# Kernel tuning notes

Hardware: AMD Instinct MI355X
Metric: run time of the kernel (lower is better)

The kernel has to match this reference:

```python
import jax, jax.numpy as jnp
import numpy as np

SCALE = 2
PAD = 4
EPS = 1e-5
K = 5
N, C, H, W = 4, 64, 128, 128


def _splits(a, s):
    # (..., W, H) -> (..., W/s, H/s, s*s), block decimation matching torch view/permute
    *lead, Wd, Hd = a.shape
    b = a.reshape(*lead, s, Wd // s, s, Hd // s)
    nl = len(lead)
    b = jnp.transpose(b, tuple(range(nl)) + (nl + 1, nl + 3, nl, nl + 2))
    return b.reshape(*lead, Wd // s, Hd // s, s * s)


def _p2o(psf, Hs, Ws):
    # PSF -> OTF: zero-pad, roll to center at origin, FFT
    kh, kw = psf.shape[-2], psf.shape[-1]
    otf = jnp.zeros(psf.shape[:-2] + (Hs, Ws), psf.dtype).at[..., :kh, :kw].set(psf)
    otf = jnp.roll(otf, (-(kh // 2), -(kw // 2)), axis=(-2, -1))
    return jnp.fft.fftn(otf, axes=(-2, -1))


def _upsample(x, s):
    # s-fold zero-filling upsampler (S^T y)
    n, c, h, w = x.shape
    return jnp.zeros((n, c, h * s, w * s), x.dtype).at[..., ::s, ::s].set(x)


def setup_inputs() -> dict:
    key = jax.random.key(0)
    kx, kw_, _ = jax.random.split(key, 3)
    x = jax.random.normal(kx, (N, C, H, W), dtype=jnp.float32)
    w_raw = jax.random.normal(kw_, (1, C, K, K), dtype=jnp.float32)
    weight = jax.nn.softmax(w_raw.reshape(1, C, -1), axis=-1).reshape(1, C, K, K)
    bias = jnp.zeros((1, C, 1, 1), dtype=jnp.float32)
    return {"x": x, "weight": weight, "bias": bias}


def reference(x, weight, bias):
    s = SCALE
    xp = jnp.pad(x, ((0, 0), (0, 0), (PAD, PAD), (PAD, PAD)), mode="wrap")  # circular
    biaseps = jax.nn.sigmoid(bias - 9.0) + EPS  # (1,C,1,1)
    _, _, h, w = xp.shape
    STy = _upsample(xp, s)  # zero-filled upsample
    # nearest-neighbor interpolate by integer factor s
    xn = jnp.repeat(jnp.repeat(xp, s, axis=-2), s, axis=-1)
    FB = _p2o(weight, h * s, w * s)           # (1,C,hs,ws) complex
    FBC = jnp.conj(FB)
    F2B = jnp.abs(FB) ** 2                     # real
    FBFy = FBC * jnp.fft.fftn(STy, axes=(-2, -1))
    FR = FBFy + jnp.fft.fftn(biaseps * xn, axes=(-2, -1))
    x1 = FB * FR
    FBR = jnp.mean(_splits(x1, s), axis=-1)    # (N,C,h,w) complex
    invW = jnp.mean(_splits(F2B, s), axis=-1)  # (1,C,h,w) real
    invWBR = FBR / (invW + biaseps)
    FCBinvWBR = FBC * jnp.tile(invWBR, (1, 1, s, s))
    FX = (FR - FCBinvWBR) / biaseps
    out = jnp.real(jnp.fft.ifftn(FX, axes=(-2, -1)))
    out = out[..., PAD * s:-PAD * s, PAD * s:-PAD * s]
    return out
```

## Files before the change

kernel.cpp:

```cpp
#include <hip/hip_runtime.h>
#include <math.h>


#define MDIM 136
#define RSC  70
#define HC   69
#define PLANE_HALF (MDIM*HC)
#define NPLANES 256
#define LDS_CPLX2 (2*MDIM*RSC + 2*MDIM + 2*119 + 2*51)
#define PI_D 3.14159265358979323846
#define NTH 1024

__device__ __forceinline__ int slot136(int k) { return 17*(k & 7) + (k >> 3); }
__device__ __forceinline__ int slot68(int k)  { return 17*(k & 3) + (k >> 2); }

template<int DIR, class F>
__device__ __forceinline__ void dft17_sink(float2* z, int base, int stride, F f)
{
    constexpr float C17[9] = {1.f, 0.93247223f, 0.73900892f, 0.44573836f,
                              0.09226836f, -0.27366299f, -0.60263464f,
                              -0.85021714f, -0.98297310f};
    constexpr float S17[9] = {0.f, 0.36124167f, 0.67369564f, 0.89516329f,
                              0.99573418f, 0.96182564f, 0.79801723f,
                              0.52643216f, 0.18374952f};
    constexpr float d = (DIR > 0) ? 1.f : -1.f;
    float xr[17], xi[17];
#pragma unroll
    for (int n = 0; n < 17; n++) {
        float2 v = z[base + n*stride];
        xr[n] = v.x; xi[n] = v.y;
    }
    float ar[8], ai[8], br[8], bi[8];
#pragma unroll
    for (int n = 1; n <= 8; n++) {
        ar[n-1] = xr[n] + xr[17-n];  ai[n-1] = xi[n] + xi[17-n];
        br[n-1] = xr[n] - xr[17-n];  bi[n-1] = xi[n] - xi[17-n];
    }
    float s0r = xr[0], s0i = xi[0];
#pragma unroll
    for (int n = 0; n < 8; n++) { s0r += ar[n]; s0i += ai[n]; }
    f(0, s0r, s0i);
#pragma unroll
    for (int k = 1; k <= 8; k++) {
        float Pr = xr[0], Pi = xi[0], Qr = 0.f, Qi = 0.f;
#pragma unroll
        for (int n = 1; n <= 8; n++) {
            int m = (k*n) % 17;
            float cc = (m <= 8) ? C17[m] : C17[17-m];
            float ss = (m <= 8) ? S17[m] : -S17[17-m];
            Pr = fmaf(ar[n-1], cc, Pr);
            Pi = fmaf(ai[n-1], cc, Pi);
            Qr = fmaf(br[n-1], ss, Qr);
            Qi = fmaf(bi[n-1], ss, Qi);
        }
        f(k,    Pr - d*Qi, Pi + d*Qr);
        f(17-k, Pr + d*Qi, Pi - d*Qr);
    }
}

template<int DIR>
__device__ __forceinline__ void radix4_tw(float2* z, const float2* t68, int base, int n2,
                                          float2 Z0, float2 Z1, float2 Z2, float2 Z3)
{
    constexpr float d = (DIR > 0) ? 1.0f : -1.0f;
    float t0r = Z0.x+Z2.x, t0i = Z0.y+Z2.y;
    float t1r = Z0.x-Z2.x, t1i = Z0.y-Z2.y;
    float t2r = Z1.x+Z3.x, t2i = Z1.y+Z3.y;
    float t3r = Z1.x-Z3.x, t3i = Z1.y-Z3.y;
    float X0r = t0r+t2r,     X0i = t0i+t2i;
    float X2r = t0r-t2r,     X2i = t0i-t2i;
    float X1r = t1r - d*t3i, X1i = t1i + d*t3r;
    float X3r = t1r + d*t3i, X3i = t1i - d*t3r;
    z[base + n2] = make_float2(X0r, X0i);
    float2 w1 = t68[n2], w2 = t68[17 + n2], w3 = t68[34 + n2];
    z[base + 17 + n2] = make_float2(X1r*w1.x - X1i*w1.y, X1r*w1.y + X1i*w1.x);
    z[base + 34 + n2] = make_float2(X2r*w2.x - X2i*w2.y, X2r*w2.y + X2i*w2.x);
    z[base + 51 + n2] = make_float2(X3r*w3.x - X3i*w3.y, X3r*w3.y + X3i*w3.x);
}

template<int DIR>
__device__ __forceinline__ void fft136_s1_body(float2* z, const float2* t136,
                                               int c, int n2)
{
    constexpr float d = (DIR > 0) ? 1.0f : -1.0f;
    constexpr float C707 = 0.70710678118654752f;
    float xr[8], xi[8];
#pragma unroll
    for (int n1 = 0; n1 < 8; n1++) {
        float2 v = z[(17*n1 + n2)*RSC + c];
        xr[n1] = v.x; xi[n1] = v.y;
    }
    float e0r = xr[0]+xr[4], e0i = xi[0]+xi[4];
    float e1r = xr[0]-xr[4], e1i = xi[0]-xi[4];
    float o0r = xr[2]+xr[6], o0i = xi[2]+xi[6];
    float o1r = xr[2]-xr[6], o1i = xi[2]-xi[6];
    float E0r = e0r+o0r, E0i = e0i+o0i;
    float E2r = e0r-o0r, E2i = e0i-o0i;
    float E1r = e1r - d*o1i, E1i = e1i + d*o1r;
    float E3r = e1r + d*o1i, E3i = e1i - d*o1r;
    float f0r = xr[1]+xr[5], f0i = xi[1]+xi[5];
    float f1r = xr[1]-xr[5], f1i = xi[1]-xi[5];
    float h0r = xr[3]+xr[7], h0i = xi[3]+xi[7];
    float h1r = xr[3]-xr[7], h1i = xi[3]-xi[7];
    float O0r = f0r+h0r, O0i = f0i+h0i;
    float O2r = f0r-h0r, O2i = f0i-h0i;
    float O1r = f1r - d*h1i, O1i = f1i + d*h1r;
    float O3r = f1r + d*h1i, O3i = f1i - d*h1r;
    float t1r =  C707*(O1r - d*O1i), t1i = C707*(O1i + d*O1r);
    float t2r = -d*O2i,              t2i = d*O2r;
    float t3r = -C707*(O3r + d*O3i), t3i = C707*(d*O3r - O3i);
    float Xr[8], Xi[8];
    Xr[0]=E0r+O0r; Xi[0]=E0i+O0i;  Xr[4]=E0r-O0r; Xi[4]=E0i-O0i;
    Xr[1]=E1r+t1r; Xi[1]=E1i+t1i;  Xr[5]=E1r-t1r; Xi[5]=E1i-t1i;
    Xr[2]=E2r+t2r; Xi[2]=E2i+t2i;  Xr[6]=E2r-t2r; Xi[6]=E2i-t2i;
    Xr[3]=E3r+t3r; Xi[3]=E3i+t3i;  Xr[7]=E3r-t3r; Xi[7]=E3i-t3i;
    z[n2*RSC + c] = make_float2(Xr[0], Xi[0]);
#pragma unroll
    for (int k1 = 1; k1 < 8; k1++) {
        float2 w = t136[(k1-1)*17 + n2];
        z[(17*k1 + n2)*RSC + c] = make_float2(Xr[k1]*w.x - Xi[k1]*w.y,
                                              Xr[k1]*w.y + Xi[k1]*w.x);
    }
}

template<int DIR>
__device__ void fft136_s1(float2* z, const float2* t136, int ncols, int tid)
{
    int c = tid / 17;
    int n2 = tid - c*17;
    for (int e = tid; e < ncols*17; e += NTH) {
        fft136_s1_body<DIR>(z, t136, c, n2);
        c += 60; n2 += 4; if (n2 >= 17) { n2 -= 17; c++; }
    }
}

template<int DIR>
__device__ void ct68_s1(float2* z, const float2* t68, int tid)
{
    int row = tid / 17;
    int n2  = tid - row*17;
    for (int e = tid; e < MDIM*17; e += NTH) {
        int base = row*RSC;
        float2 Z0 = z[base + n2];
        float2 Z1 = z[base + 17 + n2];
        float2 Z2 = z[base + 34 + n2];
        float2 Z3 = z[base + 51 + n2];
        radix4_tw<DIR>(z, t68, base, n2, Z0, Z1, Z2, Z3);
        row += 60; n2 += 4; if (n2 >= 17) { n2 -= 17; row++; }
    }
}

__device__ __forceinline__ float2 c2r_pack(float2 a, float2 b, float2 w)
{
    float Sr = a.x + b.x, Si = a.y - b.y;
    float Dr = a.x - b.x, Di = a.y + b.y;
    float Or = w.x*Dr - w.y*Di, Oi = w.x*Di + w.y*Dr;
    return make_float2(Sr - Oi, Si + Or);
}

__global__ __launch_bounds__(1024, 4) void conv_kernel(const float* __restrict__ x,
                                                       const float2* __restrict__ Abuf,
                                                       float* __restrict__ out)
{
    extern __shared__ float2 zsm[];
    float2* z0    = zsm;
    float2* z1    = zsm + MDIM*RSC;
    float2* lutI  = zsm + 2*MDIM*RSC;
    float2* lutF  = lutI + MDIM;
    float2* tI136 = lutF + MDIM;
    float2* tF136 = tI136 + 119;
    float2* tI68  = tF136 + 119;
    float2* tF68  = tI68 + 51;
    const int tid = threadIdx.x;
    const int nc  = blockIdx.x;
    const int c   = nc & 63;

    if (tid < MDIM) {
        float s, cc; sincosf(2.0f*(float)PI_D*(float)tid/136.0f, &s, &cc);
        lutI[tid] = make_float2(cc, s);
        lutF[tid] = make_float2(cc, -s);
    } else if (tid < MDIM + 119) {
        int it = tid - MDIM;
        int k1 = it/17 + 1, n2 = it - (it/17)*17;
        float s, cc; sincosf((float)(PI_D/68.0)*(float)(k1*n2), &s, &cc);
        tI136[it] = make_float2(cc, s);
        tF136[it] = make_float2(cc, -s);
    } else if (tid < MDIM + 119 + 51) {
        int it = tid - MDIM - 119;
        int j = it/17, n2 = it - 17*j;
        float s, cc; sincosf((float)(PI_D/34.0)*(float)((j+1)*n2), &s, &cc);
        tI68[it] = make_float2(cc, s);
        tF68[it] = make_float2(cc, -s);
    }
    const float* xp = x + (size_t)nc * (128*128);
    {
        int i = tid / 68, n = tid - (tid/68)*68;
        for (int e = tid; e < MDIM*68; e += NTH) {
            int si = (i + 124) & 127;
            int j0 = (2*n + 124) & 127;
            z0[i*RSC + n] = *reinterpret_cast<const float2*>(xp + si*128 + j0);
            i += 15; n += 4; if (n >= 68) { n -= 68; i++; }
        }
    }
    __syncthreads();
    ct68_s1<-1>(z0, tF68, tid);
    __syncthreads();
    if (tid < MDIM*4) {
        int row = tid >> 2, k1 = tid & 3;
        int base = row*RSC + 17*k1;
        dft17_sink<-1>(z0, base, 1, [&](int k2, float re, float im) {
            z0[base + k2] = make_float2(re, im);
        });
    }
    __syncthreads();
    {
        int row = tid / 35, k = tid - (tid/35)*35;
        for (int e = tid; e < MDIM*35; e += NTH) {
            int base = row*RSC;
            int sa = slot68(k);
            float2 Za = z0[base+sa];
            float Zar = Za.x, Zai = Za.y;
            float Zbr, Zbi; int sb;
            if (k == 0) { Zbr = Zar; Zbi = Zai; sb = 68; }
            else {
                int kk = 68-k; sb = slot68(kk);
                float2 Zb = z0[base+sb]; Zbr = Zb.x; Zbi = Zb.y;
            }
            float2 w = lutF[k];
            float wc = w.x, ws = w.y;
            float Er = 0.5f*(Zar + Zbr), Ei = 0.5f*(Zai - Zbi);
            float Dr = 0.5f*(Zar - Zbr), Di = 0.5f*(Zai + Zbi);
            float Tr = wc*Dr - ws*Di, Ti = wc*Di + ws*Dr;
            z0[base+sa] = make_float2(Er + Ti, Ei - Tr);
            float E2r = Er,  E2i = -Ei;
            float D2r = -Dr, D2i = Di;
            float w2c = -wc, w2s = ws;
            float T2r = w2c*D2r - w2s*D2i, T2i = w2c*D2i + w2s*D2r;
            z0[base+sb] = make_float2(E2r + T2i, E2i - T2r);
            row += 29; k += 9; if (k >= 35) { k -= 35; row++; }
        }
    }
    __syncthreads();
    float2 Ar0[10], Ar1[10];
    {
        const float2* A0 = Abuf + (size_t)(c*4) * PLANE_HALF;
        const float2* A1 = A0 + PLANE_HALF;
        int e = tid;
#pragma unroll
        for (int k = 0; k < 10; k++) {
            if (k < 9 || tid < PLANE_HALF - 9*NTH) { Ar0[k] = A0[e]; Ar1[k] = A1[e]; }
            e += NTH;
        }
    }
    fft136_s1<-1>(z0, tF136, HC, tid);
    __syncthreads();
    if (tid < HC*8) {
        int cc = tid >> 3, k1 = tid & 7;
        int base = 17*k1*RSC + cc;
        dft17_sink<-1>(z0, base, RSC, [&](int k2, float re, float im) {
            z0[base + k2*RSC] = make_float2(re, im);
        });
    }
    __syncthreads();
    float2 Xreg[10];
    {
        int g1 = tid / HC, g2 = tid - (tid/HC)*HC;
#pragma unroll
        for (int k = 0; k < 10; k++) {
            if (k < 9 || tid < PLANE_HALF - 9*NTH) {
                int cq = (g2 == 68) ? 68 : slot68(g2);
                Xreg[k] = z0[slot136(g1)*RSC + cq];
            }
            g1 += 14; g2 += 58; if (g2 >= HC) { g2 -= HC; g1++; }
        }
    }
    __syncthreads();
    float* op = out + (size_t)nc * (256*256);
#pragma unroll 1
    for (int u = 0; u < 2; u++) {
        {
            int g1 = tid / HC, g2 = tid - (tid/HC)*HC;
#pragma unroll
            for (int k = 0; k < 10; k++) {
                if (k < 9 || tid < PLANE_HALF - 9*NTH) {
                    float2 xv = Xreg[k];
                    float2 a0 = Ar0[k], a1 = Ar1[k];
                    int a = g1*RSC + g2;
                    z0[a] = make_float2(a0.x*xv.x - a0.y*xv.y, a0.x*xv.y + a0.y*xv.x);
                    z1[a] = make_float2(a1.x*xv.x - a1.y*xv.y, a1.x*xv.y + a1.y*xv.x);
                }
                g1 += 14; g2 += 58; if (g2 >= HC) { g2 -= HC; g1++; }
            }
        }
        __syncthreads();
        if (u == 0) {
            const float2* A0 = Abuf + (size_t)(c*4 + 2) * PLANE_HALF;
            const float2* A1 = A0 + PLANE_HALF;
            int e = tid;
#pragma unroll
            for (int k = 0; k < 10; k++) {
                if (k < 9 || tid < PLANE_HALF - 9*NTH) { Ar0[k] = A0[e]; Ar1[k] = A1[e]; }
                e += NTH;
            }
        }
        for (int it = tid; it < 2*HC*17; it += NTH) {
            int pl = it >= HC*17;
            int ee = it - (pl ? HC*17 : 0);
            int cc = (ee*241) >> 12;
            int n2 = ee - cc*17;
            fft136_s1_body<1>(pl ? z1 : z0, tI136, cc, n2);
        }
        __syncthreads();
        for (int it = tid; it < 2*HC*8; it += NTH) {
            int pl = it >= HC*8;
            int i  = it - (pl ? HC*8 : 0);
            float2* zz = pl ? z1 : z0;
            int cc = i >> 3, k1 = i & 7;
            int base = 17*k1*RSC + cc;
            dft17_sink<1>(zz, base, RSC, [&](int k2, float re, float im) {
                zz[base + k2*RSC] = make_float2(re, im);
            });
        }
        __syncthreads();
        for (int it = tid; it < 2*MDIM*9; it += NTH) {
            int pl = it >= MDIM*9;
            int i  = it - (pl ? MDIM*9 : 0);
            float2* zz = pl ? z1 : z0;
            int row = (i*7282) >> 16;
            int g   = i - row*9;
            int base = row*RSC;
            if (g == 0) {
                float2 T0  = zz[base],    T17 = zz[base+17], T34 = zz[base+34],
                       T51 = zz[base+51], T68 = zz[base+68];
                float2 Z0 = c2r_pack(T0,  T68, lutI[0]);
                float2 Z1 = c2r_pack(T17, T51, lutI[17]);
                float2 Z2 = c2r_pack(T34, T34, lutI[34]);
                float2 Z3 = c2r_pack(T51, T17, lutI[51]);
                radix4_tw<1>(zz, tI68, base, 0, Z0, Z1, Z2, Z3);
            } else {
                int gb = 17 - g;
                float2 Ta0 = zz[base+g],    Ta1 = zz[base+g+17],
                       Ta2 = zz[base+g+34], Ta3 = zz[base+g+51];
                float2 Tb0 = zz[base+gb],    Tb1 = zz[base+gb+17],
                       Tb2 = zz[base+gb+34], Tb3 = zz[base+gb+51];
                float2 Za0 = c2r_pack(Ta0, Tb3, lutI[g]);
                float2 Za1 = c2r_pack(Ta1, Tb2, lutI[g+17]);
                float2 Za2 = c2r_pack(Ta2, Tb1, lutI[g+34]);
                float2 Za3 = c2r_pack(Ta3, Tb0, lutI[g+51]);
                float2 Zb0 = c2r_pack(Tb0, Ta3, lutI[gb]);
                float2 Zb1 = c2r_pack(Tb1, Ta2, lutI[gb+17]);
                float2 Zb2 = c2r_pack(Tb2, Ta1, lutI[gb+34]);
                float2 Zb3 = c2r_pack(Tb3, Ta0, lutI[gb+51]);
                radix4_tw<1>(zz, tI68, base, g,  Za0, Za1, Za2, Za3);
                radix4_tw<1>(zz, tI68, base, gb, Zb0, Zb1, Zb2, Zb3);
            }
        }
        __syncthreads();
        for (int it = tid; it < 2*MDIM*4; it += NTH) {
            int pl = it >= MDIM*4;
            int i  = it - (pl ? MDIM*4 : 0);
            float2* zz = pl ? z1 : z0;
            int row = i >> 2, k1 = i & 3;
            int base = row*RSC + 17*k1;
            dft17_sink<1>(zz, base, 1, [&](int k2, float re, float im) {
                zz[base + k2] = make_float2(re, im);
            });
        }
        __syncthreads();
        {
            int m  = 2 + (tid & 63);
            int y1 = 4 + (tid >> 6);
            int a  = slot136(y1)*RSC + slot68(m);
            float* rowp = op + (size_t)(2*y1 + u - 8)*256 + 4*m - 8;
#pragma unroll
            for (int it = 0; it < 8; ++it) {
                float2 w0 = z0[a], w1 = z1[a];
                *reinterpret_cast<float4*>(rowp) = make_float4(w0.x, w1.x, w0.y, w1.y);
                a += 2*RSC;
                rowp += 32*256;
            }
        }
        __syncthreads();
    }
}

__global__ void prep_kernel(const float* __restrict__ weight,
                            const float* __restrict__ bias,
                            float2* __restrict__ Abuf)
{
    __shared__ double tabc[272], tabs[272];
    __shared__ double Rs[69*5*4];
    for (int t = threadIdx.x; t < 272; t += blockDim.x) {
        double s, c; sincos(-2.0*PI_D*(double)t/272.0, &s, &c);
        tabc[t] = c; tabs[t] = s;
    }
    const int c     = blockIdx.x >> 3;
    const int chunk = blockIdx.x & 7;
    const float* wp = weight + c*25;
    const double r = 1.0/(1.0 + exp(9.0 - (double)bias[c])) + 1e-5;
    __syncthreads();
    for (int it = threadIdx.x; it < 69*5; it += blockDim.x) {
        int g2 = it / 5, a = it - 5*g2;
        double c2 = tabc[g2], s2 = tabs[g2];
        double e2r[5], e2i[5];
        e2r[2]=1.0; e2i[2]=0.0; e2r[3]=c2; e2i[3]=s2;
        e2r[4]=c2*c2-s2*s2; e2i[4]=2.0*c2*s2;
        e2r[1]=c2; e2i[1]=-s2; e2r[0]=e2r[4]; e2i[0]=-e2i[4];
        double w0=wp[a*5+0], w1=wp[a*5+1], w2=wp[a*5+2], w3=wp[a*5+3], w4=wp[a*5+4];
        double Rer = w0*e2r[0] + w2*e2r[2] + w4*e2r[4];
        double Rei = w0*e2i[0] + w2*e2i[2] + w4*e2i[4];
        double Ror = w1*e2r[1] + w3*e2r[3];
        double Roi = w1*e2i[1] + w3*e2i[3];
        Rs[it*4+0] = Rer + Ror;  Rs[it*4+1] = Rei + Roi;
        Rs[it*4+2] = Rer - Ror;  Rs[it*4+3] = Rei - Roi;
    }
    __syncthreads();

    const int e_lo = chunk * 1173;
    const int e_hi = e_lo + 1173;
    int e  = e_lo + (int)threadIdx.x;
    int g1 = e / HC, g2 = e - (e/HC)*HC;
    for (; e < e_hi; e += blockDim.x) {
        double c1 = tabc[g1], s1 = tabs[g1];
        double e1r[5], e1i[5];
        e1r[2]=1.0; e1i[2]=0.0; e1r[3]=c1; e1i[3]=s1;
        e1r[4]=c1*c1-s1*s1; e1i[4]=2.0*c1*s1;
        e1r[1]=c1; e1i[1]=-s1; e1r[0]=e1r[4]; e1i[0]=-e1i[4];

        double FBr[2][2], FBi[2][2];
#pragma unroll
        for (int b1 = 0; b1 < 2; b1++) {
            double Per=0, Pei=0, Por=0, Poi=0;
#pragma unroll
            for (int a = 0; a < 5; a++) {
                double Rr = Rs[(g2*5+a)*4 + 2*b1];
                double Ri = Rs[(g2*5+a)*4 + 2*b1 + 1];
                double tr = e1r[a]*Rr - e1i[a]*Ri;
                double ti = e1r[a]*Ri + e1i[a]*Rr;
                if (a & 1) { Por += tr; Poi += ti; } else { Per += tr; Pei += ti; }
            }
            FBr[0][b1] = Per + Por;  FBi[0][b1] = Pei + Poi;
            FBr[1][b1] = Per - Por;  FBi[1][b1] = Pei - Poi;
        }
        double c2 = tabc[g2], s2 = tabs[g2];
        double ur[2]={1.0+c1, 1.0-c1}, ui[2]={s1, -s1};
        double vr[2]={1.0+c2, 1.0-c2}, vi[2]={s2, -s2};
        double Br_[2][2], Bi_[2][2];
#pragma unroll
        for (int a1 = 0; a1 < 2; a1++)
#pragma unroll
            for (int b1 = 0; b1 < 2; b1++) {
                Br_[a1][b1] = ur[a1]*vr[b1] - ui[a1]*vi[b1];
                Bi_[a1][b1] = ur[a1]*vi[b1] + ui[a1]*vr[b1];
            }
        double invW=0, Qr=0, Qi=0;
#pragma unroll
        for (int a1 = 0; a1 < 2; a1++)
#pragma unroll
            for (int b1 = 0; b1 < 2; b1++) {
                invW += FBr[a1][b1]*FBr[a1][b1] + FBi[a1][b1]*FBi[a1][b1];
                Qr += FBr[a1][b1]*Br_[a1][b1] - FBi[a1][b1]*Bi_[a1][b1];
                Qi += FBr[a1][b1]*Bi_[a1][b1] + FBi[a1][b1]*Br_[a1][b1];
            }
        invW *= 0.25; Qr *= 0.25; Qi *= 0.25;
        double den = 1.0/(invW + r);
        double Sr = (1.0 - Qr)*den, Si = -Qi*den;
        double Mr[2][2], Mi[2][2];
#pragma unroll
        for (int a1 = 0; a1 < 2; a1++)
#pragma unroll
            for (int b1 = 0; b1 < 2; b1++) {
                Mr[a1][b1] = Br_[a1][b1] + FBr[a1][b1]*Sr + FBi[a1][b1]*Si;
                Mi[a1][b1] = Bi_[a1][b1] + FBr[a1][b1]*Si - FBi[a1][b1]*Sr;
            }
        const double scale = 1.0/73984.0;
#pragma unroll
        for (int uu = 0; uu < 2; uu++)
#pragma unroll
            for (int vv = 0; vv < 2; vv++) {
                double sr=0, si=0;
#pragma unroll
                for (int a1 = 0; a1 < 2; a1++)
#pragma unroll
                    for (int b1 = 0; b1 < 2; b1++) {
                        if ((a1*uu + b1*vv) & 1) { sr -= Mr[a1][b1]; si -= Mi[a1][b1]; }
                        else                     { sr += Mr[a1][b1]; si += Mi[a1][b1]; }
                    }
                int t = g1*uu + g2*vv;
                double pc = tabc[t], ps = -tabs[t];
                float2 outv;
                outv.x = (float)((pc*sr - ps*si)*scale);
                outv.y = (float)((pc*si + ps*sr)*scale);
                Abuf[((size_t)(c*4 + uu*2 + vv))*PLANE_HALF + e] = outv;
            }
        g1 += 3; g2 += 49; if (g2 >= HC) { g2 -= HC; g1++; }
    }
}

extern "C" void kernel_launch(void* const* d_in, const int* in_sizes, int n_in,
                              void* d_out, int out_size, void* d_ws, size_t ws_size,
                              hipStream_t stream)
{
    const float* x      = (const float*)d_in[0];
    const float* weight = (const float*)d_in[1];
    const float* bias   = (const float*)d_in[2];
    float* out = (float*)d_out;

    float2* Abuf = (float2*)d_ws;

    const size_t lds_conv = (size_t)LDS_CPLX2 * sizeof(float2);
    (void)hipFuncSetAttribute((const void*)conv_kernel,
                              hipFuncAttributeMaxDynamicSharedMemorySize, (int)lds_conv);

    prep_kernel<<<512, 256, 0, stream>>>(weight, bias, Abuf);
    conv_kernel<<<NPLANES, 1024, lds_conv, stream>>>(x, Abuf, out);
}
```

Before: 153.8 us.

## Interleave the two inverse-FFT planes into float4 LDS layout

The two output-phase planes (v=0,1) are stored interleaved as one float4 per element in LDS and in the precomputed filter buffer, instead of two separate float2 planes. The inverse FFT stages then process both planes in a single pass with 128-bit LDS accesses, which halves the number of butterfly iterations and index computations. Filter coefficients are now loaded from global memory as float4 inside the u loop rather than prefetched into registers, which lowers register pressure but exposes that load latency. The forward FFT keeps using the first half of the same buffer through a float2 view with a doubled row stride.

```diff
diff --git a/kernel.cpp b/kernel.cpp
--- a/kernel.cpp
+++ b/kernel.cpp
@@ -3,16 +3,32 @@
 
 
 #define MDIM 136
-#define RSC  70
+#define RSCF 140
+#define RSC4 70
 #define HC   69
 #define PLANE_HALF (MDIM*HC)
 #define NPLANES 256
-#define LDS_CPLX2 (2*MDIM*RSC + 2*MDIM + 2*119 + 2*51)
+#define LDS_BYTES (MDIM*RSC4*16 + 612*8)
 #define PI_D 3.14159265358979323846
 #define NTH 1024
 
 __device__ __forceinline__ int slot136(int k) { return 17*(k & 7) + (k >> 3); }
 __device__ __forceinline__ int slot68(int k)  { return 17*(k & 3) + (k >> 2); }
+
+__device__ __forceinline__ float4 q_add(float4 a, float4 b)
+{ return make_float4(a.x+b.x, a.y+b.y, a.z+b.z, a.w+b.w); }
+__device__ __forceinline__ float4 q_sub(float4 a, float4 b)
+{ return make_float4(a.x-b.x, a.y-b.y, a.z-b.z, a.w-b.w); }
+__device__ __forceinline__ float4 q_muli(float4 a, float d)
+{ return make_float4(-d*a.y, d*a.x, -d*a.w, d*a.z); }
+__device__ __forceinline__ float4 q_scale(float4 a, float s)
+{ return make_float4(s*a.x, s*a.y, s*a.z, s*a.w); }
+__device__ __forceinline__ float4 q_fma(float4 a, float s, float4 acc)
+{ return make_float4(fmaf(a.x,s,acc.x), fmaf(a.y,s,acc.y),
+                     fmaf(a.z,s,acc.z), fmaf(a.w,s,acc.w)); }
+__device__ __forceinline__ float4 cmul4(float4 q, float2 w)
+{ return make_float4(q.x*w.x - q.y*w.y, q.x*w.y + q.y*w.x,
+                     q.z*w.x - q.w*w.y, q.z*w.y + q.w*w.x); }
 
 template<int DIR, class F>
 __device__ __forceinline__ void dft17_sink(float2* z, int base, int stride, F f)
@@ -55,6 +71,46 @@
         }
         f(k,    Pr - d*Qi, Pi + d*Qr);
         f(17-k, Pr + d*Qi, Pi - d*Qr);
+    }
+}
+
+template<int DIR>
+__device__ __forceinline__ void dft17q(float4* z, int base, int stride)
+{
+    constexpr float C17[9] = {1.f, 0.93247223f, 0.73900892f, 0.44573836f,
+                              0.09226836f, -0.27366299f, -0.60263464f,
+                              -0.85021714f, -0.98297310f};
+    constexpr float S17[9] = {0.f, 0.36124167f, 0.67369564f, 0.89516329f,
+                              0.99573418f, 0.96182564f, 0.79801723f,
+                              0.52643216f, 0.18374952f};
+    constexpr float d = (DIR > 0) ? 1.f : -1.f;
+    float4 x0 = z[base];
+    float4 a[8], b[8];
+#pragma unroll
+    for (int n = 1; n <= 8; n++) {
+        float4 u = z[base + n*stride];
+        float4 v = z[base + (17-n)*stride];
+        a[n-1] = q_add(u, v);
+        b[n-1] = q_sub(u, v);
+    }
+    float4 s0 = x0;
+#pragma unroll
+    for (int n = 0; n < 8; n++) s0 = q_add(s0, a[n]);
+    z[base] = s0;
+#pragma unroll
+    for (int k = 1; k <= 8; k++) {
+        float4 P = x0, Q = make_float4(0.f,0.f,0.f,0.f);
+#pragma unroll
+        for (int n = 1; n <= 8; n++) {
+            int m = (k*n) % 17;
+            float cc = (m <= 8) ? C17[m] : C17[17-m];
+            float ss = (m <= 8) ? S17[m] : -S17[17-m];
+            P = q_fma(a[n-1], cc, P);
+            Q = q_fma(b[n-1], ss, Q);
+        }
+        float4 iq = q_muli(Q, d);
+        z[base + k*stride]      = q_add(P, iq);
+        z[base + (17-k)*stride] = q_sub(P, iq);
     }
 }
 
@@ -79,6 +135,23 @@
 }
 
 template<int DIR>
+__device__ __forceinline__ void radix4q_tw(float4* z, const float2* t68, int base, int n2,
+                                           float4 Z0, float4 Z1, float4 Z2, float4 Z3)
+{
+    constexpr float d = (DIR > 0) ? 1.0f : -1.0f;
+    float4 t0 = q_add(Z0, Z2), t1 = q_sub(Z0, Z2);
+    float4 t2 = q_add(Z1, Z3), t3 = q_sub(Z1, Z3);
+    float4 X0 = q_add(t0, t2), X2 = q_sub(t0, t2);
+    float4 it3 = q_muli(t3, d);
+    float4 X1 = q_add(t1, it3), X3 = q_sub(t1, it3);
+    z[base + n2] = X0;
+    float2 w1 = t68[n2], w2 = t68[17 + n2], w3 = t68[34 + n2];
+    z[base + 17 + n2] = cmul4(X1, w1);
+    z[base + 34 + n2] = cmul4(X2, w2);
+    z[base + 51 + n2] = cmul4(X3, w3);
+}
+
+template<int DIR>
 __device__ __forceinline__ void fft136_s1_body(float2* z, const float2* t136,
                                                int c, int n2)
 {
@@ -87,7 +160,7 @@
     float xr[8], xi[8];
 #pragma unroll
     for (int n1 = 0; n1 < 8; n1++) {
-        float2 v = z[(17*n1 + n2)*RSC + c];
+        float2 v = z[(17*n1 + n2)*RSCF + c];
         xr[n1] = v.x; xi[n1] = v.y;
     }
     float e0r = xr[0]+xr[4], e0i = xi[0]+xi[4];
@@ -114,40 +187,49 @@
     Xr[1]=E1r+t1r; Xi[1]=E1i+t1i;  Xr[5]=E1r-t1r; Xi[5]=E1i-t1i;
     Xr[2]=E2r+t2r; Xi[2]=E2i+t2i;  Xr[6]=E2r-t2r; Xi[6]=E2i-t2i;
     Xr[3]=E3r+t3r; Xi[3]=E3i+t3i;  Xr[7]=E3r-t3r; Xi[7]=E3i-t3i;
-    z[n2*RSC + c] = make_float2(Xr[0], Xi[0]);
+    z[n2*RSCF + c] = make_float2(Xr[0], Xi[0]);
 #pragma unroll
     for (int k1 = 1; k1 < 8; k1++) {
         float2 w = t136[(k1-1)*17 + n2];
-        z[(17*k1 + n2)*RSC + c] = make_float2(Xr[k1]*w.x - Xi[k1]*w.y,
-                                              Xr[k1]*w.y + Xi[k1]*w.x);
+        z[(17*k1 + n2)*RSCF + c] = make_float2(Xr[k1]*w.x - Xi[k1]*w.y,
+                                               Xr[k1]*w.y + Xi[k1]*w.x);
     }
 }
 
 template<int DIR>
-__device__ void fft136_s1(float2* z, const float2* t136, int ncols, int tid)
-{
-    int c = tid / 17;
-    int n2 = tid - c*17;
-    for (int e = tid; e < ncols*17; e += NTH) {
-        fft136_s1_body<DIR>(z, t136, c, n2);
-        c += 60; n2 += 4; if (n2 >= 17) { n2 -= 17; c++; }
-    }
-}
-
-template<int DIR>
-__device__ void ct68_s1(float2* z, const float2* t68, int tid)
-{
-    int row = tid / 17;
-    int n2  = tid - row*17;
-    for (int e = tid; e < MDIM*17; e += NTH) {
-        int base = row*RSC;
-        float2 Z0 = z[base + n2];
-        float2 Z1 = z[base + 17 + n2];
-        float2 Z2 = z[base + 34 + n2];
-        float2 Z3 = z[base + 51 + n2];
-        radix4_tw<DIR>(z, t68, base, n2, Z0, Z1, Z2, Z3);
-        row += 60; n2 += 4; if (n2 >= 17) { n2 -= 17; row++; }
-    }
+__device__ __forceinline__ void fft136q_s1_body(float4* z, const float2* t136,
+                                                int c, int n2)
+{
+    constexpr float d = (DIR > 0) ? 1.0f : -1.0f;
+    constexpr float C707 = 0.70710678118654752f;
+    float4 x[8];
+#pragma unroll
+    for (int n1 = 0; n1 < 8; n1++) x[n1] = z[(17*n1 + n2)*RSC4 + c];
+    float4 e0 = q_add(x[0], x[4]), e1 = q_sub(x[0], x[4]);
+    float4 o0 = q_add(x[2], x[6]), o1 = q_sub(x[2], x[6]);
+    float4 E0 = q_add(e0, o0), E2 = q_sub(e0, o0);
+    float4 io1 = q_muli(o1, d);
+    float4 E1 = q_add(e1, io1), E3 = q_sub(e1, io1);
+    float4 f0 = q_add(x[1], x[5]), f1 = q_sub(x[1], x[5]);
+    float4 h0 = q_add(x[3], x[7]), h1 = q_sub(x[3], x[7]);
+    float4 O0 = q_add(f0, h0), O2 = q_sub(f0, h0);
+    float4 ih1 = q_muli(h1, d);
+    float4 O1 = q_add(f1, ih1), O3 = q_sub(f1, ih1);
+    float4 t1 = q_scale(q_add(O1, q_muli(O1, d)), C707);
+    float4 t2 = q_muli(O2, d);
+    float4 t3 = q_scale(q_sub(O3, q_muli(O3, d)), -C707);
+    float4 X0 = q_add(E0, O0), X4 = q_sub(E0, O0);
+    float4 X1 = q_add(E1, t1), X5 = q_sub(E1, t1);
+    float4 X2 = q_add(E2, t2), X6 = q_sub(E2, t2);
+    float4 X3 = q_add(E3, t3), X7 = q_sub(E3, t3);
+    z[n2*RSC4 + c] = X0;
+    z[(17*1 + n2)*RSC4 + c] = cmul4(X1, t136[0*17 + n2]);
+    z[(17*2 + n2)*RSC4 + c] = cmul4(X2, t136[1*17 + n2]);
+    z[(17*3 + n2)*RSC4 + c] = cmul4(X3, t136[2*17 + n2]);
+    z[(17*4 + n2)*RSC4 + c] = cmul4(X4, t136[3*17 + n2]);
+    z[(17*5 + n2)*RSC4 + c] = cmul4(X5, t136[4*17 + n2]);
+    z[(17*6 + n2)*RSC4 + c] = cmul4(X6, t136[5*17 + n2]);
+    z[(17*7 + n2)*RSC4 + c] = cmul4(X7, t136[6*17 + n2]);
 }
 
 __device__ __forceinline__ float2 c2r_pack(float2 a, float2 b, float2 w)
@@ -157,15 +239,25 @@
     float Or = w.x*Dr - w.y*Di, Oi = w.x*Di + w.y*Dr;
     return make_float2(Sr - Oi, Si + Or);
 }
+__device__ __forceinline__ float4 c2r_pack4(float4 a, float4 b, float2 w)
+{
+    float Sx = a.x + b.x, Sy = a.y - b.y;
+    float Dx = a.x - b.x, Dy = a.y + b.y;
+    float Ox = w.x*Dx - w.y*Dy, Oy = w.x*Dy + w.y*Dx;
+    float Sz = a.z + b.z, Sw = a.w - b.w;
+    float Dz = a.z - b.z, Dw = a.w + b.w;
+    float Oz = w.x*Dz - w.y*Dw, Ow = w.x*Dw + w.y*Dz;
+    return make_float4(Sx - Oy, Sy + Ox, Sz - Ow, Sw + Oz);
+}
 
 __global__ __launch_bounds__(1024, 4) void conv_kernel(const float* __restrict__ x,
-                                                       const float2* __restrict__ Abuf,
+                                                       const float4* __restrict__ Abuf,
                                                        float* __restrict__ out)
 {
-    extern __shared__ float2 zsm[];
-    float2* z0    = zsm;
-    float2* z1    = zsm + MDIM*RSC;
-    float2* lutI  = zsm + 2*MDIM*RSC;
+    extern __shared__ float4 z4s[];
+    float4* z4    = z4s;
+    float2* zf    = (float2*)z4s;
+    float2* lutI  = (float2*)(z4s + MDIM*RSC4);
     float2* lutF  = lutI + MDIM;
     float2* tI136 = lutF + MDIM;
     float2* tF136 = tI136 + 119;
@@ -198,67 +290,72 @@
         for (int e = tid; e < MDIM*68; e += NTH) {
             int si = (i + 124) & 127;
             int j0 = (2*n + 124) & 127;
-            z0[i*RSC + n] = *reinterpret_cast<const float2*>(xp + si*128 + j0);
+            zf[i*RSCF + n] = *reinterpret_cast<const float2*>(xp + si*128 + j0);
             i += 15; n += 4; if (n >= 68) { n -= 68; i++; }
         }
     }
     __syncthreads();
-    ct68_s1<-1>(z0, tF68, tid);
+    {
+        int row = tid / 17;
+        int n2  = tid - row*17;
+        for (int e = tid; e < MDIM*17; e += NTH) {
+            int base = row*RSCF;
+            float2 Z0 = zf[base + n2];
+            float2 Z1 = zf[base + 17 + n2];
+            float2 Z2 = zf[base + 34 + n2];
+            float2 Z3 = zf[base + 51 + n2];
+            radix4_tw<-1>(zf, tF68, base, n2, Z0, Z1, Z2, Z3);
+            row += 60; n2 += 4; if (n2 >= 17) { n2 -= 17; row++; }
+        }
+    }
     __syncthreads();
     if (tid < MDIM*4) {
         int row = tid >> 2, k1 = tid & 3;
-        int base = row*RSC + 17*k1;
-        dft17_sink<-1>(z0, base, 1, [&](int k2, float re, float im) {
-            z0[base + k2] = make_float2(re, im);
+        int base = row*RSCF + 17*k1;
+        dft17_sink<-1>(zf, base, 1, [&](int k2, float re, float im) {
+            zf[base + k2] = make_float2(re, im);
         });
     }
     __syncthreads();
     {
         int row = tid / 35, k = tid - (tid/35)*35;
         for (int e = tid; e < MDIM*35; e += NTH) {
-            int base = row*RSC;
+            int base = row*RSCF;
             int sa = slot68(k);
-            float2 Za = z0[base+sa];
+            float2 Za = zf[base+sa];
             float Zar = Za.x, Zai = Za.y;
             float Zbr, Zbi; int sb;
             if (k == 0) { Zbr = Zar; Zbi = Zai; sb = 68; }
             else {
                 int kk = 68-k; sb = slot68(kk);
-                float2 Zb = z0[base+sb]; Zbr = Zb.x; Zbi = Zb.y;
+                float2 Zb = zf[base+sb]; Zbr = Zb.x; Zbi = Zb.y;
             }
             float2 w = lutF[k];
             float wc = w.x, ws = w.y;
             float Er = 0.5f*(Zar + Zbr), Ei = 0.5f*(Zai - Zbi);
             float Dr = 0.5f*(Zar - Zbr), Di = 0.5f*(Zai + Zbi);
             float Tr = wc*Dr - ws*Di, Ti = wc*Di + ws*Dr;
-            z0[base+sa] = make_float2(Er + Ti, Ei - Tr);
+            zf[base+sa] = make_float2(Er + Ti, Ei - Tr);
             float E2r = Er,  E2i = -Ei;
             float D2r = -Dr, D2i = Di;
             float w2c = -wc, w2s = ws;
             float T2r = w2c*D2r - w2s*D2i, T2i = w2c*D2i + w2s*D2r;
-            z0[base+sb] = make_float2(E2r + T2i, E2i - T2r);
+            zf[base+sb] = make_float2(E2r + T2i, E2i - T2r);
             row += 29; k += 9; if (k >= 35) { k -= 35; row++; }
         }
     }
     __syncthreads();
-    float2 Ar0[10], Ar1[10];
-    {
-        const float2* A0 = Abuf + (size_t)(c*4) * PLANE_HALF;
-        const float2* A1 = A0 + PLANE_HALF;
-        int e = tid;
-#pragma unroll
-        for (int k = 0; k < 10; k++) {
-            if (k < 9 || tid < PLANE_HALF - 9*NTH) { Ar0[k] = A0[e]; Ar1[k] = A1[e]; }
-            e += NTH;
-        }
-    }
-    fft136_s1<-1>(z0, tF136, HC, tid);
+    for (int e = tid; e < HC*17; e += NTH) {
+        int cc = (e*241) >> 12;
+        int n2 = e - cc*17;
+        fft136_s1_body<-1>(zf, tF136, cc, n2);
+    }
     __syncthreads();
     if (tid < HC*8) {
         int cc = tid >> 3, k1 = tid & 7;
-        int base = 17*k1*RSC + cc;
-        dft17_sink<-1>(z0, base, RSC, [&](int k2, float re, float im) {
-            z0[base + k2*RSC] = make_float2(re, im);
+        int base = 17*k1*RSCF + cc;
+        dft17_sink<-1>(zf, base, RSCF, [&](int k2, float re, float im) {
+            zf[base + k2*RSCF] = make_float2(re, im);
         });
     }
     __syncthreads();
@@ -269,7 +366,7 @@
         for (int k = 0; k < 10; k++) {
             if (k < 9 || tid < PLANE_HALF - 9*NTH) {
                 int cq = (g2 == 68) ? 68 : slot68(g2);
-                Xreg[k] = z0[slot136(g1)*RSC + cq];
+                Xreg[k] = zf[slot136(g1)*RSCF + cq];
             }
             g1 += 14; g2 += 58; if (g2 >= HC) { g2 -= HC; g1++; }
         }
@@ -278,105 +375,79 @@
     float* op = out + (size_t)nc * (256*256);
 #pragma unroll 1
     for (int u = 0; u < 2; u++) {
+        const float4* Ap = Abuf + (size_t)(c*2 + u) * PLANE_HALF;
         {
             int g1 = tid / HC, g2 = tid - (tid/HC)*HC;
 #pragma unroll
             for (int k = 0; k < 10; k++) {
                 if (k < 9 || tid < PLANE_HALF - 9*NTH) {
                     float2 xv = Xreg[k];
-                    float2 a0 = Ar0[k], a1 = Ar1[k];
-                    int a = g1*RSC + g2;
-                    z0[a] = make_float2(a0.x*xv.x - a0.y*xv.y, a0.x*xv.y + a0.y*xv.x);
-                    z1[a] = make_float2(a1.x*xv.x - a1.y*xv.y, a1.x*xv.y + a1.y*xv.x);
+                    float4 av = Ap[tid + k*NTH];
+                    z4[g1*RSC4 + g2] = make_float4(
+                        av.x*xv.x - av.y*xv.y, av.x*xv.y + av.y*xv.x,
+                        av.z*xv.x - av.w*xv.y, av.z*xv.y + av.w*xv.x);
                 }
                 g1 += 14; g2 += 58; if (g2 >= HC) { g2 -= HC; g1++; }
             }
         }
         __syncthreads();
-        if (u == 0) {
-            const float2* A0 = Abuf + (size_t)(c*4 + 2) * PLANE_HALF;
-            const float2* A1 = A0 + PLANE_HALF;
-            int e = tid;
-#pragma unroll
-            for (int k = 0; k < 10; k++) {
-                if (k < 9 || tid < PLANE_HALF - 9*NTH) { Ar0[k] = A0[e]; Ar1[k] = A1[e]; }
-                e += NTH;
-            }
-        }
-        for (int it = tid; it < 2*HC*17; it += NTH) {
-            int pl = it >= HC*17;
-            int ee = it - (pl ? HC*17 : 0);
-            int cc = (ee*241) >> 12;
-            int n2 = ee - cc*17;
-            fft136_s1_body<1>(pl ? z1 : z0, tI136, cc, n2);
+        for (int e = tid; e < HC*17; e += NTH) {
+            int cc = (e*241) >> 12;
+            int n2 = e - cc*17;
+            fft136q_s1_body<1>(z4, tI136, cc, n2);
         }
         __syncthreads();
-        for (int it = tid; it < 2*HC*8; it += NTH) {
-            int pl = it >= HC*8;
-            int i  = it - (pl ? HC*8 : 0);
-            float2* zz = pl ? z1 : z0;
-            int cc = i >> 3, k1 = i & 7;
-            int base = 17*k1*RSC + cc;
-            dft17_sink<1>(zz, base, RSC, [&](int k2, float re, float im) {
-                zz[base + k2*RSC] = make_float2(re, im);
-            });
+        if (tid < HC*8) {
+            int cc = tid >> 3, k1 = tid & 7;
+            dft17q<1>(z4, 17*k1*RSC4 + cc, RSC4);
         }
         __syncthreads();
-        for (int it = tid; it < 2*MDIM*9; it += NTH) {
-            int pl = it >= MDIM*9;
-            int i  = it - (pl ? MDIM*9 : 0);
-            float2* zz = pl ? z1 : z0;
-            int row = (i*7282) >> 16;
-            int g   = i - row*9;
-            int base = row*RSC;
+        for (int it = tid; it < MDIM*9; it += NTH) {
+            int row = (it*7282) >> 16;
+            int g   = it - row*9;
+            int base = row*RSC4;
             if (g == 0) {
-                float2 T0  = zz[base],    T17 = zz[base+17], T34 = zz[base+34],
-                       T51 = zz[base+51], T68 = zz[base+68];
-                float2 Z0 = c2r_pack(T0,  T68, lutI[0]);
-                float2 Z1 = c2r_pack(T17, T51, lutI[17]);
-                float2 Z2 = c2r_pack(T34, T34, lutI[34]);
-                float2 Z3 = c2r_pack(T51, T17, lutI[51]);
-                radix4_tw<1>(zz, tI68, base, 0, Z0, Z1, Z2, Z3);
+                float4 T0  = z4[base],    T17 = z4[base+17], T34 = z4[base+34],
+                       T51 = z4[base+51], T68 = z4[base+68];
+                float4 Z0 = c2r_pack4(T0,  T68, lutI[0]);
+                float4 Z1 = c2r_pack4(T17, T51, lutI[17]);
+                float4 Z2 = c2r_pack4(T34, T34, lutI[34]);
+                float4 Z3 = c2r_pack4(T51, T17, lutI[51]);
+                radix4q_tw<1>(z4, tI68, base, 0, Z0, Z1, Z2, Z3);
             } else {
                 int gb = 17 - g;
-                float2 Ta0 = zz[base+g],    Ta1 = zz[base+g+17],
-                       Ta2 = zz[base+g+34], Ta3 = zz[base+g+51];
-                float2 Tb0 = zz[base+gb],    Tb1 = zz[base+gb+17],
-                       Tb2 = zz[base+gb+34], Tb3 = zz[base+gb+51];
-                float2 Za0 = c2r_pack(Ta0, Tb3, lutI[g]);
-                float2 Za1 = c2r_pack(Ta1, Tb2, lutI[g+17]);
-                float2 Za2 = c2r_pack(Ta2, Tb1, lutI[g+34]);
-                float2 Za3 = c2r_pack(Ta3, Tb0, lutI[g+51]);
-                float2 Zb0 = c2r_pack(Tb0, Ta3, lutI[gb]);
-                float2 Zb1 = c2r_pack(Tb1, Ta2, lutI[gb+17]);
-                float2 Zb2 = c2r_pack(Tb2, Ta1, lutI[gb+34]);
-                float2 Zb3 = c2r_pack(Tb3, Ta0, lutI[gb+51]);
-                radix4_tw<1>(zz, tI68, base, g,  Za0, Za1, Za2, Za3);
-                radix4_tw<1>(zz, tI68, base, gb, Zb0, Zb1, Zb2, Zb3);
+                float4 Ta0 = z4[base+g],    Ta1 = z4[base+g+17],
+                       Ta2 = z4[base+g+34], Ta3 = z4[base+g+51];
+                float4 Tb0 = z4[base+gb],    Tb1 = z4[base+gb+17],
+                       Tb2 = z4[base+gb+34], Tb3 = z4[base+gb+51];
+                float4 Za0 = c2r_pack4(Ta0, Tb3, lutI[g]);
+                float4 Za1 = c2r_pack4(Ta1, Tb2, lutI[g+17]);
+                float4 Za2 = c2r_pack4(Ta2, Tb1, lutI[g+34]);
+                float4 Za3 = c2r_pack4(Ta3, Tb0, lutI[g+51]);
+                float4 Zb0 = c2r_pack4(Tb0, Ta3, lutI[gb]);
+                float4 Zb1 = c2r_pack4(Tb1, Ta2, lutI[gb+17]);
+                float4 Zb2 = c2r_pack4(Tb2, Ta1, lutI[gb+34]);
+                float4 Zb3 = c2r_pack4(Tb3, Ta0, lutI[gb+51]);
+                radix4q_tw<1>(z4, tI68, base, g,  Za0, Za1, Za2, Za3);
+                radix4q_tw<1>(z4, tI68, base, gb, Zb0, Zb1, Zb2, Zb3);
             }
         }
         __syncthreads();
-        for (int it = tid; it < 2*MDIM*4; it += NTH) {
-            int pl = it >= MDIM*4;
-            int i  = it - (pl ? MDIM*4 : 0);
-            float2* zz = pl ? z1 : z0;
-            int row = i >> 2, k1 = i & 3;
-            int base = row*RSC + 17*k1;
-            dft17_sink<1>(zz, base, 1, [&](int k2, float re, float im) {
-                zz[base + k2] = make_float2(re, im);
-            });
+        if (tid < MDIM*4) {
+            int row = tid >> 2, k1 = tid & 3;
+            dft17q<1>(z4, row*RSC4 + 17*k1, 1);
         }
         __syncthreads();
         {
             int m  = 2 + (tid & 63);
             int y1 = 4 + (tid >> 6);
-            int a  = slot136(y1)*RSC + slot68(m);
+            int a  = slot136(y1)*RSC4 + slot68(m);
             float* rowp = op + (size_t)(2*y1 + u - 8)*256 + 4*m - 8;
 #pragma unroll
             for (int it = 0; it < 8; ++it) {
-                float2 w0 = z0[a], w1 = z1[a];
-                *reinterpret_cast<float4*>(rowp) = make_float4(w0.x, w1.x, w0.y, w1.y);
-                a += 2*RSC;
+                float4 w = z4[a];
+                *reinterpret_cast<float4*>(rowp) = make_float4(w.x, w.z, w.y, w.w);
+                a += 2*RSC4;
                 rowp += 32*256;
             }
         }
@@ -386,7 +457,7 @@
 
 __global__ void prep_kernel(const float* __restrict__ weight,
                             const float* __restrict__ bias,
-                            float2* __restrict__ Abuf)
+                            float4* __restrict__ Abuf)
 {
     __shared__ double tabc[272], tabs[272];
     __shared__ double Rs[69*5*4];
@@ -475,7 +546,8 @@
             }
         const double scale = 1.0/73984.0;
 #pragma unroll
-        for (int uu = 0; uu < 2; uu++)
+        for (int uu = 0; uu < 2; uu++) {
+            float ov[4];
 #pragma unroll
             for (int vv = 0; vv < 2; vv++) {
                 double sr=0, si=0;
@@ -488,11 +560,12 @@
                     }
                 int t = g1*uu + g2*vv;
                 double pc = tabc[t], ps = -tabs[t];
-                float2 outv;
-                outv.x = (float)((pc*sr - ps*si)*scale);
-                outv.y = (float)((pc*si + ps*sr)*scale);
-                Abuf[((size_t)(c*4 + uu*2 + vv))*PLANE_HALF + e] = outv;
-            }
+                ov[2*vv]   = (float)((pc*sr - ps*si)*scale);
+                ov[2*vv+1] = (float)((pc*si + ps*sr)*scale);
+            }
+            Abuf[((size_t)(c*2 + uu))*PLANE_HALF + e] =
+                make_float4(ov[0], ov[1], ov[2], ov[3]);
+        }
         g1 += 3; g2 += 49; if (g2 >= HC) { g2 -= HC; g1++; }
     }
 }
@@ -506,12 +579,12 @@
     const float* bias   = (const float*)d_in[2];
     float* out = (float*)d_out;
 
-    float2* Abuf = (float2*)d_ws;
-
-    const size_t lds_conv = (size_t)LDS_CPLX2 * sizeof(float2);
+    float4* Abuf = (float4*)d_ws;
+
     (void)hipFuncSetAttribute((const void*)conv_kernel,
-                              hipFuncAttributeMaxDynamicSharedMemorySize, (int)lds_conv);
+                              hipFuncAttributeMaxDynamicSharedMemorySize,
+                              (int)LDS_BYTES);
 
     prep_kernel<<<512, 256, 0, stream>>>(weight, bias, Abuf);
-    conv_kernel<<<NPLANES, 1024, lds_conv, stream>>>(x, Abuf, out);
-}
+    conv_kernel<<<NPLANES, 1024, LDS_BYTES, stream>>>(x, Abuf, out);
+}
```

After: 141.5 us. 8.0% less time.
